# Performance work log

Measured on AMD Instinct MI355X. Metric: run time of the kernel, lower is better.

## Reference

```python
import jax, jax.numpy as jnp
import numpy as np

FP8 = jnp.float8_e4m3fn
FP8_MAX = 448.0  # float8_e4m3fn max finite value used by the module


def setup_inputs() -> dict:
    key = jax.random.key(0)
    k1, k2, k3 = jax.random.split(key, 3)
    x = jax.random.normal(k1, (4096, 4096), dtype=jnp.float32)          # [tokens, in_features]
    weight = jax.random.normal(k2, (16384, 4096), dtype=jnp.float32) * 0.02  # [out, in] fp32 master weight
    bias = jax.random.normal(k3, (16384,), dtype=jnp.float32) * 0.01
    return {"x": x, "weight": weight, "bias": bias}


def reference(x, weight, bias):
    # quantize_weight: per-tensor scale from fp32 weight, cast to fp8 (saturating)
    w_scale = FP8_MAX / (jnp.max(jnp.abs(weight)) + 1e-6)
    w_fp8 = (weight * w_scale).astype(FP8)
    # quantize_activation: per-tensor dynamic scale
    x_abs_max = jnp.max(jnp.abs(x)) + 1e-6
    x_scale = FP8_MAX / x_abs_max
    x_fp8 = (x * x_scale).astype(FP8)
    # upcast fp8 -> fp32 matmul, then descale + bias (same as torch module)
    out = jnp.matmul(x_fp8.astype(jnp.float32), w_fp8.astype(jnp.float32).T)
    out = out / (x_scale * w_scale)
    out = out + bias
    return out.astype(FP8)
```

## Files before the change

kernel.cpp:

```cpp
#include <hip/hip_runtime.h>
#include <math.h>
#include <stdint.h>

#define TOK  4096
#define KIN  4096
#define NOUT 16384

#define BM 128
#define BN 128
#define BK 64
#define NT (KIN / BK)

#define FBM 64
#define FBN 64
#define FBK 32
#define FLDP (FBK + 2)

typedef int int32x4  __attribute__((ext_vector_type(4)));
typedef int int32x16 __attribute__((ext_vector_type(16)));

__global__ void init_ws_kernel(unsigned int* hdr) {
  if (threadIdx.x < 2) hdr[threadIdx.x] = 0u;
}

__global__ void absmax_kernel(const float4* __restrict__ src, int n4,
                              unsigned int* __restrict__ dst) {
  float m = 0.0f;
  for (int i = blockIdx.x * blockDim.x + threadIdx.x; i < n4;
       i += gridDim.x * blockDim.x) {
    float4 v = src[i];
    m = fmaxf(m, fmaxf(fmaxf(fabsf(v.x), fabsf(v.y)),
                       fmaxf(fabsf(v.z), fabsf(v.w))));
  }
#pragma unroll
  for (int off = 32; off > 0; off >>= 1) m = fmaxf(m, __shfl_down(m, off, 64));
  __shared__ float sm[4];
  if ((threadIdx.x & 63) == 0) sm[threadIdx.x >> 6] = m;
  __syncthreads();
  if (threadIdx.x == 0) {
    m = fmaxf(fmaxf(sm[0], sm[1]), fmaxf(sm[2], sm[3]));
    atomicMax(dst, __float_as_uint(m));
  }
}

__device__ __forceinline__ float scale_f32(unsigned int maxbits) {
  return __fdiv_rn(448.0f, __fadd_rn(__uint_as_float(maxbits), 1e-6f));
}

__device__ __forceinline__ unsigned char enc_fp8_f32(float v) {
  unsigned char s = (v < 0.0f) ? 0x80 : 0x00;
  float a = fabsf(v);
  if (a == 0.0f) return s;
  int e2;
  (void)frexpf(a, &e2);
  int p = e2 - 4;
  if (p < -9) p = -9;
  int n = (int)rintf(ldexpf(a, -p));
  if (n == 16) { n = 8; p += 1; }
  int E, mm;
  if (n >= 8) { E = p + 10; mm = n - 8; }
  else        { E = 0;      mm = n;     }
  return (unsigned char)(s | (E << 3) | mm);
}

__device__ __forceinline__ double out_value(double v) {
  if (v == 0.0) return 0.0;
  double a = fabs(v);
  int e2;
  (void)frexp(a, &e2);
  int p = e2 - 4;
  if (p < -9) p = -9;
  double t = ldexp(a, -p);
  double r;
  if (p <= -2) {
    r = ldexp(floor(t) + 0.5, p);
  } else {
    int n = (int)rint(t);
    if (n == 16) { n = 8; p += 1; }
    r = ldexp((double)n, p);
  }
  return (v < 0.0) ? -r : r;
}

__global__ void encode_kernel(const float* __restrict__ src, int n,
                              const unsigned int* __restrict__ maxbits,
                              unsigned char* __restrict__ codes) {
  const float scale = scale_f32(*maxbits);
  for (int i = blockIdx.x * blockDim.x + threadIdx.x; i < n;
       i += gridDim.x * blockDim.x) {
    codes[i] = enc_fp8_f32(__fmul_rn(src[i], scale));
  }
}

__global__ void encode_digits_kernel(const float4* __restrict__ src, int n4,
                                     const unsigned int* __restrict__ maxbits,
                                     unsigned int* __restrict__ p0,
                                     unsigned int* __restrict__ p1,
                                     unsigned int* __restrict__ p2) {
  const float scale = scale_f32(*maxbits);
  for (int i = blockIdx.x * blockDim.x + threadIdx.x; i < n4;
       i += gridDim.x * blockDim.x) {
    float4 v = src[i];
    const float f[4] = {v.x, v.y, v.z, v.w};
    unsigned int b0 = 0, b1 = 0, b2 = 0;
#pragma unroll
    for (int j = 0; j < 4; ++j) {
      unsigned char c = enc_fp8_f32(__fmul_rn(f[j], scale));
      int E = (c >> 3) & 15, mm = c & 7;
      int mag = E ? ((8 + mm) << (E - 1)) : mm;
      int iv = (c & 0x80) ? -mag : mag;
      int d0 = ((iv + 64) & 127) - 64;
      int t1 = (iv - d0) >> 7;
      int d1 = ((t1 + 64) & 127) - 64;
      int d2 = (t1 - d1) >> 7;
      b0 |= (unsigned int)(d0 & 255) << (8 * j);
      b1 |= (unsigned int)(d1 & 255) << (8 * j);
      b2 |= (unsigned int)(d2 & 255) << (8 * j);
    }
    p0[i] = b0; p1[i] = b1; p2[i] = b2;
  }
}

__device__ __forceinline__ void glds16(const void* g, void* l) {
  __builtin_amdgcn_global_load_lds(
      (const __attribute__((address_space(1))) void*)g,
      (__attribute__((address_space(3))) void*)l, 16, 0, 0);
}

__global__ __launch_bounds__(512, 2) void gemm_i8_kernel(
    const int8_t* __restrict__ xd, const int8_t* __restrict__ wd,
    const float* __restrict__ bias, const unsigned int* __restrict__ hdr,
    float* __restrict__ out) {
  constexpr int PLANE = BM * BK;
  constexpr int BUF   = 6 * PLANE;
  __shared__ __attribute__((aligned(16))) int8_t lds[3 * BUF];

  const int tid  = threadIdx.x;
  const int lane = tid & 63;
  const int wv   = tid >> 6;
  const int wm   = wv >> 1;
  const int wn   = wv & 1;

  const int bid = (int)blockIdx.x;
  const int xcd = bid & 7;
  const int c   = bid >> 3;
  const int m0  = (c & 31) * BM;
  const int n0  = ((xcd << 4) + (c >> 5)) * BN;

  const int srow = lane >> 2;
  const int su   = (lane & 3) ^ ((lane >> 3) & 3);
  const int8_t* asrc = xd + (size_t)(m0 + wv * 16 + srow) * KIN + su * 16;
  const int8_t* bsrc = wd + (size_t)(n0 + wv * 16 + srow) * KIN + su * 16;
  const size_t XPL = (size_t)TOK * KIN;
  const size_t WPL = (size_t)NOUT * KIN;

  const int arow  = wm * 32 + (lane & 31);
  const int aoff  = arow * BK + ((((lane >> 5) ^ (arow >> 1)) & 3) << 4);
  const int brow0 = wn * 64 + (lane & 31);
  const int brow1 = brow0 + 32;
  const int boff0 = brow0 * BK + ((((lane >> 5) ^ (brow0 >> 1)) & 3) << 4);
  const int boff1 = brow1 * BK + ((((lane >> 5) ^ (brow1 >> 1)) & 3) << 4);

  int32x16 acc[2][5] = {};

  auto STAGE = [&](int buf, int t) {
    int8_t* lb = lds + buf * BUF + wv * 1024;
    const int k0 = t * BK;
#pragma unroll
    for (int p = 0; p < 3; ++p) {
      glds16(asrc + p * XPL + k0, lb + p * PLANE);
      glds16(bsrc + p * WPL + k0, lb + (3 + p) * PLANE);
    }
  };

  STAGE(0, 0);
  STAGE(1, 1);

  int cur = 0, stg = 2;
  for (int t = 0; t < NT; ++t) {
    if (t + 1 < NT) asm volatile("s_waitcnt vmcnt(6)" ::: "memory");
    else            asm volatile("s_waitcnt vmcnt(0)" ::: "memory");
    __builtin_amdgcn_s_barrier();
    __builtin_amdgcn_sched_barrier(0);
    if (t + 2 < NT) STAGE(stg, t + 2);
    __builtin_amdgcn_sched_barrier(0);

    const int8_t* lb = lds + cur * BUF;
#pragma unroll
    for (int kk = 0; kk < 2; ++kk) {
      const int kx = kk << 5;
      int32x4 af[3], bf0[3], bf1[3];
#pragma unroll
      for (int p = 0; p < 3; ++p) {
        af[p]  = *(const int32x4*)(lb + p * PLANE + (aoff ^ kx));
        bf0[p] = *(const int32x4*)(lb + (3 + p) * PLANE + (boff0 ^ kx));
        bf1[p] = *(const int32x4*)(lb + (3 + p) * PLANE + (boff1 ^ kx));
      }
      __builtin_amdgcn_s_setprio(1);
#pragma unroll
      for (int pa = 0; pa < 3; ++pa)
#pragma unroll
        for (int pb = 0; pb < 3; ++pb) {
          acc[0][pa + pb] = __builtin_amdgcn_mfma_i32_32x32x32_i8(
              af[pa], bf0[pb], acc[0][pa + pb], 0, 0, 0);
          acc[1][pa + pb] = __builtin_amdgcn_mfma_i32_32x32x32_i8(
              af[pa], bf1[pb], acc[1][pa + pb], 0, 0, 0);
        }
      __builtin_amdgcn_s_setprio(0);
    }
    cur = (cur == 2) ? 0 : cur + 1;
    stg = (stg == 2) ? 0 : stg + 1;
  }

  const float xs  = scale_f32(hdr[0]);
  const float wsc = scale_f32(hdr[1]);
  const double denom = (double)__fmul_rn(xs, wsc);

#pragma unroll
  for (int s = 0; s < 2; ++s) {
    const int n = n0 + wn * 64 + s * 32 + (lane & 31);
    const double bn = (double)bias[n];
#pragma unroll
    for (int r = 0; r < 16; ++r) {
      const int m = m0 + wm * 32 + (r & 3) + 8 * (r >> 2) + 4 * (lane >> 5);
      double S = (double)acc[s][0][r]
               + 128.0       * (double)acc[s][1][r]
               + 16384.0     * (double)acc[s][2][r]
               + 2097152.0   * (double)acc[s][3][r]
               + 268435456.0 * (double)acc[s][4][r];
      double tt = S * 0x1p-18;
      tt = tt / denom;
      tt += bn;
      out[(size_t)m * NOUT + n] = (float)out_value(tt);
    }
  }
}

__global__ __launch_bounds__(256) void gemm_fp64_kernel(
    const uint8_t* __restrict__ xq, const uint8_t* __restrict__ wq,
    const float* __restrict__ bias, const unsigned int* __restrict__ hdr,
    float* __restrict__ out) {
  __shared__ double As[FBM][FLDP];
  __shared__ double Bs[FBN][FLDP];
  __shared__ float lut[256];

  const int tid = threadIdx.x;
  {
    int E = (tid >> 3) & 15, mm = tid & 7;
    float mag = E ? ldexpf((float)(8 + mm), E - 10) : ldexpf((float)mm, -9);
    lut[tid] = (tid & 0x80) ? -mag : mag;
  }
  const float xs  = scale_f32(hdr[0]);
  const float wsc = scale_f32(hdr[1]);
  const double denom = (double)__fmul_rn(xs, wsc);

  const int m0 = blockIdx.y * FBM;
  const int n0 = blockIdx.x * FBN;
  const int r  = tid >> 2;
  const int cb = (tid & 3) * 8;
  const int rt = tid >> 4;
  const int ct = tid & 15;

  double acc[4][4] = {{0.0}};
  const uint8_t* pa = xq + (size_t)(m0 + r) * KIN + cb;
  const uint8_t* pb = wq + (size_t)(n0 + r) * KIN + cb;

  __syncthreads();
  for (int k0 = 0; k0 < KIN; k0 += FBK) {
    uint2 ua = *(const uint2*)(pa + k0);
    uint2 ub = *(const uint2*)(pb + k0);
    unsigned wa0 = ua.x, wa1 = ua.y, wb0 = ub.x, wb1 = ub.y;
#pragma unroll
    for (int b = 0; b < 4; b++) {
      As[r][cb + b]     = (double)lut[(wa0 >> (8 * b)) & 255];
      As[r][cb + 4 + b] = (double)lut[(wa1 >> (8 * b)) & 255];
      Bs[r][cb + b]     = (double)lut[(wb0 >> (8 * b)) & 255];
      Bs[r][cb + 4 + b] = (double)lut[(wb1 >> (8 * b)) & 255];
    }
    __syncthreads();
#pragma unroll 8
    for (int kk = 0; kk < FBK; kk++) {
      double a[4], bb[4];
#pragma unroll
      for (int i = 0; i < 4; i++) a[i] = As[rt + 16 * i][kk];
#pragma unroll
      for (int j = 0; j < 4; j++) bb[j] = Bs[ct + 16 * j][kk];
#pragma unroll
      for (int i = 0; i < 4; i++)
#pragma unroll
        for (int j = 0; j < 4; j++)
          acc[i][j] = fma(a[i], bb[j], acc[i][j]);
    }
    __syncthreads();
  }

#pragma unroll
  for (int i = 0; i < 4; i++) {
    const int m = m0 + rt + 16 * i;
#pragma unroll
    for (int j = 0; j < 4; j++) {
      const int n = n0 + ct + 16 * j;
      double t = acc[i][j] / denom;
      t += (double)bias[n];
      out[(size_t)m * NOUT + n] = (float)out_value(t);
    }
  }
}

extern "C" void kernel_launch(void* const* d_in, const int* in_sizes, int n_in,
                              void* d_out, int out_size, void* d_ws,
                              size_t ws_size, hipStream_t stream) {
  const float* x    = (const float*)d_in[0];
  const float* w    = (const float*)d_in[1];
  const float* bias = (const float*)d_in[2];
  float* out        = (float*)d_out;

  unsigned int* hdr = (unsigned int*)d_ws;

  hipLaunchKernelGGL(init_ws_kernel, dim3(1), dim3(64), 0, stream, hdr);
  hipLaunchKernelGGL(absmax_kernel, dim3(1024), dim3(256), 0, stream,
                     (const float4*)x, TOK * KIN / 4, hdr + 0);
  hipLaunchKernelGGL(absmax_kernel, dim3(2048), dim3(256), 0, stream,
                     (const float4*)w, NOUT * KIN / 4, hdr + 1);

  const size_t TOKK = (size_t)TOK * KIN;
  const size_t NK   = (size_t)NOUT * KIN;
  const size_t need = 64 + 3 * TOKK + 3 * NK;

  if (ws_size >= need) {
    int8_t* xd = (int8_t*)d_ws + 64;
    int8_t* wd = xd + 3 * TOKK;
    hipLaunchKernelGGL(encode_digits_kernel, dim3(2048), dim3(256), 0, stream,
                       (const float4*)x, (int)(TOKK / 4), hdr + 0,
                       (unsigned int*)xd,
                       (unsigned int*)(xd + TOKK),
                       (unsigned int*)(xd + 2 * TOKK));
    hipLaunchKernelGGL(encode_digits_kernel, dim3(4096), dim3(256), 0, stream,
                       (const float4*)w, (int)(NK / 4), hdr + 1,
                       (unsigned int*)wd,
                       (unsigned int*)(wd + NK),
                       (unsigned int*)(wd + 2 * NK));
    hipLaunchKernelGGL(gemm_i8_kernel,
                       dim3((NOUT / BN) * (TOK / BM)), dim3(512), 0, stream,
                       xd, wd, bias, hdr, out);
  } else {
    uint8_t* xq = (uint8_t*)d_ws + 64;
    uint8_t* wq = xq + TOKK;
    hipLaunchKernelGGL(encode_kernel, dim3(2048), dim3(256), 0, stream, x,
                       TOK * KIN, hdr + 0, xq);
    hipLaunchKernelGGL(encode_kernel, dim3(4096), dim3(256), 0, stream, w,
                       NOUT * KIN, hdr + 1, wq);
    hipLaunchKernelGGL(gemm_fp64_kernel, dim3(NOUT / FBN, TOK / FBM),
                       dim3(256), 0, stream, xq, wq, bias, hdr, out);
  }
}
```

Before: 2.455 ms.

## Shrink GEMM tile to 64x128 with 256 threads, double buffering, grouped block swizzle

Changes the int8 digit-GEMM block tile from 128x128 (8 waves, triple-buffered LDS) to 64x128 (4 waves, double-buffered), with each wave staging more B rows. The block-to-tile mapping becomes a grouped swizzle for L2 locality, and pipelining drops to one stage ahead behind a plain __syncthreads. The intent is smaller LDS per block and more resident blocks. In exchange it loses A/B reuse per tile and prefetch depth, which may expose memory latency.

```diff
diff --git a/kernel.cpp b/kernel.cpp
--- a/kernel.cpp
+++ b/kernel.cpp
@@ -6,10 +6,14 @@
 #define KIN  4096
 #define NOUT 16384
 
-#define BM 128
+#define BM 64
 #define BN 128
 #define BK 64
 #define NT (KIN / BK)
+#define APL 4096
+#define BPL 8192
+#define BOFFS 12288
+#define BUF 36864
 
 #define FBM 64
 #define FBN 64
@@ -127,13 +131,11 @@
       (__attribute__((address_space(3))) void*)l, 16, 0, 0);
 }
 
-__global__ __launch_bounds__(512, 2) void gemm_i8_kernel(
+__global__ __launch_bounds__(256, 2) void gemm_i8_kernel(
     const int8_t* __restrict__ xd, const int8_t* __restrict__ wd,
     const float* __restrict__ bias, const unsigned int* __restrict__ hdr,
     float* __restrict__ out) {
-  constexpr int PLANE = BM * BK;
-  constexpr int BUF   = 6 * PLANE;
-  __shared__ __attribute__((aligned(16))) int8_t lds[3 * BUF];
+  __shared__ __attribute__((aligned(16))) int8_t lds[2 * BUF];
 
   const int tid  = threadIdx.x;
   const int lane = tid & 63;
@@ -144,13 +146,15 @@
   const int bid = (int)blockIdx.x;
   const int xcd = bid & 7;
   const int c   = bid >> 3;
-  const int m0  = (c & 31) * BM;
-  const int n0  = ((xcd << 4) + (c >> 5)) * BN;
+  const int g   = c >> 6;
+  const int i   = c & 63;
+  const int m0  = (((g & 3) << 4) + (i & 15)) * BM;
+  const int n0  = (((xcd << 4) + ((g >> 2) << 2) + (i >> 4))) * BN;
 
   const int srow = lane >> 2;
   const int su   = (lane & 3) ^ ((lane >> 3) & 3);
   const int8_t* asrc = xd + (size_t)(m0 + wv * 16 + srow) * KIN + su * 16;
-  const int8_t* bsrc = wd + (size_t)(n0 + wv * 16 + srow) * KIN + su * 16;
+  const int8_t* bsrc = wd + (size_t)(n0 + wv * 32 + srow) * KIN + su * 16;
   const size_t XPL = (size_t)TOK * KIN;
   const size_t WPL = (size_t)NOUT * KIN;
 
@@ -164,25 +168,25 @@
   int32x16 acc[2][5] = {};
 
   auto STAGE = [&](int buf, int t) {
-    int8_t* lb = lds + buf * BUF + wv * 1024;
+    int8_t* lb = lds + buf * BUF;
     const int k0 = t * BK;
 #pragma unroll
+    for (int p = 0; p < 3; ++p)
+      glds16(asrc + p * XPL + k0, lb + p * APL + wv * 1024);
+#pragma unroll
     for (int p = 0; p < 3; ++p) {
-      glds16(asrc + p * XPL + k0, lb + p * PLANE);
-      glds16(bsrc + p * WPL + k0, lb + (3 + p) * PLANE);
+      glds16(bsrc + p * WPL + k0,
+             lb + BOFFS + p * BPL + wv * 2048);
+      glds16(bsrc + p * WPL + k0 + (size_t)16 * KIN,
+             lb + BOFFS + p * BPL + wv * 2048 + 1024);
     }
   };
 
   STAGE(0, 0);
-  STAGE(1, 1);
-
-  int cur = 0, stg = 2;
+  int cur = 0;
   for (int t = 0; t < NT; ++t) {
-    if (t + 1 < NT) asm volatile("s_waitcnt vmcnt(6)" ::: "memory");
-    else            asm volatile("s_waitcnt vmcnt(0)" ::: "memory");
-    __builtin_amdgcn_s_barrier();
-    __builtin_amdgcn_sched_barrier(0);
-    if (t + 2 < NT) STAGE(stg, t + 2);
+    __syncthreads();
+    if (t + 1 < NT) STAGE(cur ^ 1, t + 1);
     __builtin_amdgcn_sched_barrier(0);
 
     const int8_t* lb = lds + cur * BUF;
@@ -192,9 +196,9 @@
       int32x4 af[3], bf0[3], bf1[3];
 #pragma unroll
       for (int p = 0; p < 3; ++p) {
-        af[p]  = *(const int32x4*)(lb + p * PLANE + (aoff ^ kx));
-        bf0[p] = *(const int32x4*)(lb + (3 + p) * PLANE + (boff0 ^ kx));
-        bf1[p] = *(const int32x4*)(lb + (3 + p) * PLANE + (boff1 ^ kx));
+        af[p]  = *(const int32x4*)(lb + p * APL + (aoff ^ kx));
+        bf0[p] = *(const int32x4*)(lb + BOFFS + p * BPL + (boff0 ^ kx));
+        bf1[p] = *(const int32x4*)(lb + BOFFS + p * BPL + (boff1 ^ kx));
       }
       __builtin_amdgcn_s_setprio(1);
 #pragma unroll
@@ -208,8 +212,7 @@
         }
       __builtin_amdgcn_s_setprio(0);
     }
-    cur = (cur == 2) ? 0 : cur + 1;
-    stg = (stg == 2) ? 0 : stg + 1;
+    cur ^= 1;
   }
 
   const float xs  = scale_f32(hdr[0]);
@@ -341,7 +344,7 @@
                        (unsigned int*)(wd + NK),
                        (unsigned int*)(wd + 2 * NK));
     hipLaunchKernelGGL(gemm_i8_kernel,
-                       dim3((NOUT / BN) * (TOK / BM)), dim3(512), 0, stream,
+                       dim3((TOK / BM) * (NOUT / BN)), dim3(256), 0, stream,
                        xd, wd, bias, hdr, out);
   } else {
     uint8_t* xq = (uint8_t*)d_ws + 64;
```

New measurement: 2.394 ms. 2.5% less time.
